# Kernel tuning notes

Hardware: AMD Instinct MI355X
Metric: run time of the kernel (lower is better)

The kernel has to match this reference:

```python
import jax, jax.numpy as jnp
import numpy as np

EMB = 1024
HEADS = 8
BUCKET = 64      # bucket_size
N_HASHES = 8


def setup_inputs() -> dict:
    key = jax.random.key(0)
    k0, k1, k2, k3, k4 = jax.random.split(key, 5)
    b, t, e = 2, 4096, EMB
    dh = e // HEADS
    n_buckets = t // BUCKET
    s = 1.0 / np.sqrt(e)
    return {
        "x": jax.random.normal(k0, (b, t, e), jnp.float32),
        "w_qk": jax.random.normal(k1, (e, e), jnp.float32) * s,
        "w_v": jax.random.normal(k2, (e, e), jnp.float32) * s,
        "w_out": jax.random.normal(k3, (e, e), jnp.float32) * s,
        "b_out": jnp.zeros((e,), jnp.float32),
        # LSH random rotations (shared across the batch, as in the TF module
        # with random_rotations_per_head=False): (dim_head, n_hashes, n_buckets//2)
        "rotations": jax.random.normal(k4, (dh, N_HASHES, n_buckets // 2), jnp.float32),
    }


def _lsh_attention(qk, v, rotations):
    # qk, v: (B, t, d) with B = batch*heads
    B, t, d = qk.shape
    nh = N_HASHES
    bucket = BUCKET
    n_buckets = t // bucket
    n_bins = n_buckets

    # ---- hash vectors ----
    rotated = jnp.einsum('btf,fhi->bhti', qk, rotations)      # (B, nh, t, nb/2)
    rotated = jnp.concatenate([rotated, -rotated], axis=-1)   # (B, nh, t, nb)
    buckets = jnp.argmax(rotated, axis=-1)                    # (B, nh, t)
    offsets = (jnp.arange(nh) * n_buckets)[None, :, None]
    buckets = (buckets + offsets).reshape(B, nh * t)          # (B, nh*t)

    # ---- sort by (bucket, position) ----
    ticker = jnp.arange(nh * t)
    buckets_and_t = t * buckets + (ticker % t)[None, :]
    sticker = jnp.argsort(buckets_and_t, axis=-1, stable=True)    # sort permutation
    undo_sort = jnp.argsort(sticker, axis=-1, stable=True)
    st = sticker % t                                              # token indices

    sqk = jnp.take_along_axis(qk, st[:, :, None], axis=1)         # (B, nh*t, d)
    sv = jnp.take_along_axis(v, st[:, :, None], axis=1)

    bq_t = st.reshape(B, nh * n_bins, bucket)
    bqk = sqk.reshape(B, nh * n_bins, bucket, d)
    bv = sv.reshape(B, nh * n_bins, bucket, d)

    bq = bqk
    # tf.math.l2_normalize with default epsilon 1e-12
    sq = jnp.maximum(jnp.sum(bqk * bqk, axis=-1, keepdims=True), 1e-12)
    bk = bqk * jax.lax.rsqrt(sq)

    def look_one_back(x):
        # x: (B, nh*n_bins, bucket[, d]) -> concat previous bin along window axis
        x1 = x.reshape((B, nh, n_bins) + x.shape[2:])
        x_extra = jnp.concatenate([x1[:, :, 1:2], x1[:, :, :-1]], axis=2)
        x_extra = x_extra.reshape(x.shape)
        return jnp.concatenate([x, x_extra], axis=2)

    bk = look_one_back(bk)        # (B, nh*n_bins, 2*bucket, d)
    bv = look_one_back(bv)
    bkv_t = look_one_back(bq_t)   # (B, nh*n_bins, 2*bucket)

    scale = d ** (-0.5)
    dots = jnp.einsum('bhie,bhje->bhij', bq * scale, bk)  # (B, nh*n_bins, bucket, 2*bucket)

    # self-attention mask (token attending to itself gets -1e5)
    self_mask = (bq_t[:, :, :, None] == bkv_t[:, :, None, :]).astype(dots.dtype)
    dots = dots * (1.0 - self_mask) + self_mask * (-1e5)

    dots_logsumexp = jax.scipy.special.logsumexp(dots, axis=-1, keepdims=True)
    probs = jnp.exp(dots - dots_logsumexp)
    bo = jnp.einsum('buij,buje->buie', probs, bv)          # (B, nh*n_bins, bucket, d)

    so = bo.reshape(B, nh * t, d)
    slogits = dots_logsumexp.reshape(B, nh * t)

    # unsort back to original token order
    o = jnp.take_along_axis(so, undo_sort[:, :, None], axis=1)
    logits = jnp.take_along_axis(slogits, undo_sort, axis=1)

    # combine the n_hashes rounds with softmax over per-round logsumexp logits
    o = o.reshape(B, nh, t, d)
    logits = logits.reshape(B, nh, t, 1)
    w = jnp.exp(logits - jax.scipy.special.logsumexp(logits, axis=1, keepdims=True))
    return jnp.sum(o * w, axis=1)  # (B, t, d)


def reference(x, w_qk, w_v, w_out, b_out, rotations):
    b, t, e = x.shape
    h = HEADS
    dh = e // h
    qk = x @ w_qk
    v = x @ w_v

    def merge_heads(z):
        return z.reshape(b, t, h, dh).transpose(0, 2, 1, 3).reshape(b * h, t, dh)

    out = _lsh_attention(merge_heads(qk), merge_heads(v), rotations)
    out = out.reshape(b, h, t, dh).transpose(0, 2, 1, 3).reshape(b, t, e)
    return out @ w_out + b_out
```

## Files before the change

### kernel.cpp

```cpp
#include <hip/hip_runtime.h>
#include <hip/hip_bf16.h>
#include <math.h>

#define T_LEN 4096
#define EMBD 1024
#define DH 128
#define NHASH 8
#define NHEADS 8
#define FLAG_CAP 65536
#define GAP_THRESH 2e-3f

typedef __attribute__((ext_vector_type(8))) short short8;
typedef __attribute__((ext_vector_type(16))) float f32x16;

__device__ __forceinline__ int swz(int row, int col) {
    return (row << 7) + (col ^ ((row & 7) << 3));
}
__device__ __forceinline__ int swz64(int row, int col) {
    return row * 64 + (col ^ ((row & 7) << 3));
}
__device__ __forceinline__ unsigned cvtpk(float lo, float hi) {
    unsigned r;
    asm("v_cvt_pk_bf16_f32 %0, %1, %2" : "=v"(r) : "v"(lo), "v"(hi));
    return r;
}
__device__ __forceinline__ float bfu_lo(unsigned u) {
    union { unsigned x; float f; } c; c.x = u << 16; return c.f;
}
__device__ __forceinline__ float bfu_hi(unsigned u) {
    union { unsigned x; float f; } c; c.x = u & 0xffff0000u; return c.f;
}
__device__ __forceinline__ float bfus2f(unsigned short s) {
    union { unsigned x; float f; } c; c.x = ((unsigned)s) << 16; return c.f;
}

__global__ __launch_bounds__(256) void k_prep_x(
    const float* __restrict__ x, __hip_bfloat16* __restrict__ xh,
    __hip_bfloat16* __restrict__ xl)
{
    int gid = blockIdx.x * 256 + threadIdx.x;
    for (int i = gid; i < 2097152; i += 524288) {
        float4 f = reinterpret_cast<const float4*>(x)[i];
        unsigned h01 = cvtpk(f.x, f.y), h23 = cvtpk(f.z, f.w);
        float l0 = f.x - bfu_lo(h01), l1 = f.y - bfu_hi(h01);
        float l2 = f.z - bfu_lo(h23), l3 = f.w - bfu_hi(h23);
        reinterpret_cast<uint2*>(xh)[i] = make_uint2(h01, h23);
        reinterpret_cast<uint2*>(xl)[i] = make_uint2(cvtpk(l0, l1), cvtpk(l2, l3));
    }
}

__global__ __launch_bounds__(256) void k_prep_w(
    const float* __restrict__ w0, const float* __restrict__ w1,
    const float* __restrict__ w2, __hip_bfloat16* __restrict__ wT)
{
    __shared__ float tileT[64 * 65];
    const int mat = blockIdx.x >> 8;
    const int tile = blockIdx.x & 255;
    const int tr = tile >> 4, tc = tile & 15;
    const int k0 = tr * 64, n0c = tc * 64;
    const float* w = (mat == 0) ? w0 : (mat == 1) ? w1 : w2;
    __hip_bfloat16* th = wT + (size_t)mat * 2097152;
    __hip_bfloat16* tl = th + 1048576;
    const int tid = threadIdx.x;

    #pragma unroll
    for (int i = 0; i < 4; ++i) {
        int idx = tid + i * 256;
        int row = idx >> 4, c4 = (idx & 15) * 4;
        float4 f = *reinterpret_cast<const float4*>(
            w + (size_t)(k0 + row) * 1024 + n0c + c4);
        tileT[(c4 + 0) * 65 + row] = f.x;
        tileT[(c4 + 1) * 65 + row] = f.y;
        tileT[(c4 + 2) * 65 + row] = f.z;
        tileT[(c4 + 3) * 65 + row] = f.w;
    }
    __syncthreads();
    #pragma unroll
    for (int i = 0; i < 4; ++i) {
        int idx = tid + i * 256;
        int nl = idx >> 4, kc4 = (idx & 15) * 4;
        float v0 = tileT[nl * 65 + kc4 + 0];
        float v1 = tileT[nl * 65 + kc4 + 1];
        float v2 = tileT[nl * 65 + kc4 + 2];
        float v3 = tileT[nl * 65 + kc4 + 3];
        unsigned h01 = cvtpk(v0, v1), h23 = cvtpk(v2, v3);
        float l0 = v0 - bfu_lo(h01), l1 = v1 - bfu_hi(h01);
        float l2 = v2 - bfu_lo(h23), l3 = v3 - bfu_hi(h23);
        size_t o = (size_t)(n0c + nl) * 1024 + k0 + kc4;
        *reinterpret_cast<uint2*>(th + o) = make_uint2(h01, h23);
        *reinterpret_cast<uint2*>(tl + o) = make_uint2(cvtpk(l0, l1), cvtpk(l2, l3));
    }
}

__global__ __launch_bounds__(256) void k_prep_a(
    const float* __restrict__ attn, const float* __restrict__ Sbuf,
    __hip_bfloat16* __restrict__ ah, __hip_bfloat16* __restrict__ al)
{
    int gid = blockIdx.x * 256 + threadIdx.x;
    for (int i = gid; i < 2097152; i += 524288) {
        int r = i >> 8;
        int e4 = (i & 255) * 4;
        int b = r >> 12, t = r & 4095;
        int h = e4 >> 7, d = e4 & 127;
        size_t gi = (size_t)(b * NHEADS + h) * T_LEN + t;
        float4 f = *reinterpret_cast<const float4*>(attn + gi * DH + d);
        float S = Sbuf[gi];
        f.x /= S; f.y /= S; f.z /= S; f.w /= S;
        unsigned h01 = cvtpk(f.x, f.y), h23 = cvtpk(f.z, f.w);
        float l0 = f.x - bfu_lo(h01), l1 = f.y - bfu_hi(h01);
        float l2 = f.z - bfu_lo(h23), l3 = f.w - bfu_hi(h23);
        reinterpret_cast<uint2*>(ah)[i] = make_uint2(h01, h23);
        reinterpret_cast<uint2*>(al)[i] = make_uint2(cvtpk(l0, l1), cvtpk(l2, l3));
    }
}

template <int EPI>
__global__ __launch_bounds__(256, 3) void k_gemm(
    const __hip_bfloat16* __restrict__ Xh_g, const __hip_bfloat16* __restrict__ Xl_g,
    const __hip_bfloat16* __restrict__ Wh_g, const __hip_bfloat16* __restrict__ Wl_g,
    void* __restrict__ o1v, void* __restrict__ o2v,
    float* __restrict__ rsn, const float* __restrict__ bias)
{
    __shared__ char smem[49152];
    short* Wh = (short*)smem;
    short* Wl = (short*)(smem + 16384);
    short* Xh = (short*)(smem + 32768);
    short* Xl = (short*)(smem + 40960);

    const int tid = threadIdx.x;
    const int mt = blockIdx.x >> 3;
    const int nt = blockIdx.x & 7;
    const int m0 = mt * 64, n0 = nt * 128;

    const int wave = tid >> 6, lane = tid & 63;
    const int it = wave & 1, jt2 = wave >> 1;
    const int h5 = lane >> 5;
    const int m_loc = it * 32 + (lane & 31);

    f32x16 acc[2] = {};

    for (int ks = 0; ks < 16; ++ks) {
        const int k0 = ks * 64;
        __syncthreads();
        for (int u = tid; u < 512; u += 256) {
            int row = u >> 3, blk = u & 7;
            size_t src = (size_t)(m0 + row) * 1024 + k0 + blk * 8;
            int dst = swz64(row, blk * 8);
            *reinterpret_cast<int4*>(&Xh[dst]) = *reinterpret_cast<const int4*>(Xh_g + src);
            *reinterpret_cast<int4*>(&Xl[dst]) = *reinterpret_cast<const int4*>(Xl_g + src);
        }
        for (int u = tid; u < 1024; u += 256) {
            int row = u >> 3, blk = u & 7;
            size_t src = (size_t)(n0 + row) * 1024 + k0 + blk * 8;
            int dst = swz64(row, blk * 8);
            *reinterpret_cast<int4*>(&Wh[dst]) = *reinterpret_cast<const int4*>(Wh_g + src);
            *reinterpret_cast<int4*>(&Wl[dst]) = *reinterpret_cast<const int4*>(Wl_g + src);
        }
        __syncthreads();

        #pragma unroll
        for (int kt = 0; kt < 4; ++kt) {
            int xoff = swz64(m_loc, kt * 16 + h5 * 8);
            short8 xfh = *reinterpret_cast<const short8*>(&Xh[xoff]);
            short8 xfl = *reinterpret_cast<const short8*>(&Xl[xoff]);
            #pragma unroll
            for (int jj = 0; jj < 2; ++jj) {
                int rowN = (jt2 * 2 + jj) * 32 + (lane & 31);
                int woff = swz64(rowN, kt * 16 + h5 * 8);
                short8 wfh = *reinterpret_cast<const short8*>(&Wh[woff]);
                short8 wfl = *reinterpret_cast<const short8*>(&Wl[woff]);
                acc[jj] = __builtin_amdgcn_mfma_f32_32x32x16_bf16(wfh, xfh, acc[jj], 0, 0, 0);
                acc[jj] = __builtin_amdgcn_mfma_f32_32x32x16_bf16(wfl, xfh, acc[jj], 0, 0, 0);
                acc[jj] = __builtin_amdgcn_mfma_f32_32x32x16_bf16(wfh, xfl, acc[jj], 0, 0, 0);
            }
        }
    }
    __syncthreads();

    float* osc = (float*)smem;
    #pragma unroll
    for (int jj = 0; jj < 2; ++jj) {
        int jt = jt2 * 2 + jj;
        #pragma unroll
        for (int r2 = 0; r2 < 16; ++r2) {
            int n = jt * 32 + (r2 & 3) + ((r2 >> 2) << 3) + (h5 << 2);
            osc[m_loc * 128 + (n ^ (m_loc & 28))] = acc[jj][r2];
        }
    }
    __syncthreads();

    #pragma unroll
    for (int w = 0; w < 8; ++w) {
        int lin = w * 256 + tid;
        int rowm = lin >> 5;
        int c4 = (lin & 31) * 4;
        float4 v4 = *reinterpret_cast<float4*>(&osc[rowm * 128 + (c4 ^ (rowm & 28))]);
        int r = m0 + rowm;
        if constexpr (EPI == 0) {
            float ss = v4.x * v4.x + v4.y * v4.y + v4.z * v4.z + v4.w * v4.w;
            #pragma unroll
            for (int mm = 1; mm < 32; mm <<= 1) ss += __shfl_xor(ss, mm);
            float rs = 1.0f / sqrtf(fmaxf(ss, 1e-12f));
            int b = r >> 12, t = r & 4095;
            int h = n0 >> 7;
            size_t base = ((size_t)(b * NHEADS + h) * T_LEN + t) * DH + c4;
            unsigned h01 = cvtpk(v4.x, v4.y), h23 = cvtpk(v4.z, v4.w);
            float l0 = v4.x - bfu_lo(h01), l1 = v4.y - bfu_hi(h01);
            float l2 = v4.z - bfu_lo(h23), l3 = v4.w - bfu_hi(h23);
            *reinterpret_cast<uint2*>((__hip_bfloat16*)o1v + base) = make_uint2(h01, h23);
            *reinterpret_cast<uint2*>((__hip_bfloat16*)o2v + base) =
                make_uint2(cvtpk(l0, l1), cvtpk(l2, l3));
            if ((lin & 31) == 0)
                rsn[(size_t)(b * NHEADS + h) * T_LEN + t] = rs;
        } else if constexpr (EPI == 1) {
            int b = r >> 12, t = r & 4095;
            int n = n0 + c4;
            int h = n >> 7, d = n & 127;
            size_t base = ((size_t)(b * NHEADS + h) * T_LEN + t) * DH + d;
            *reinterpret_cast<uint2*>((__hip_bfloat16*)o1v + base) =
                make_uint2(cvtpk(v4.x, v4.y), cvtpk(v4.z, v4.w));
        } else {
            int n = n0 + c4;
            float4 o;
            o.x = v4.x + bias[n + 0]; o.y = v4.y + bias[n + 1];
            o.z = v4.z + bias[n + 2]; o.w = v4.w + bias[n + 3];
            *reinterpret_cast<float4*>((float*)o1v + (size_t)r * 1024 + n) = o;
        }
    }
}

__global__ __launch_bounds__(256) void k_hash2f(
    const __hip_bfloat16* __restrict__ qkh, const __hip_bfloat16* __restrict__ qkl,
    const float* __restrict__ rot, unsigned* __restrict__ bucketArr,
    unsigned* __restrict__ counter, unsigned* __restrict__ flaglist)
{
    __shared__ float qs[8][EMBD];
    const int tok0 = blockIdx.x * 8;
    const int tid = threadIdx.x;
    const int j = 4 * tid;
    const int h = j >> 7, d = j & 127;

    #pragma unroll
    for (int tk = 0; tk < 8; ++tk) {
        int row = tok0 + tk;
        int b = row >> 12, t = row & 4095;
        size_t base = ((size_t)(b * NHEADS + h) * T_LEN + t) * DH + d;
        ushort4 h4 = *reinterpret_cast<const ushort4*>(qkh + base);
        ushort4 l4 = *reinterpret_cast<const ushort4*>(qkl + base);
        qs[tk][j + 0] = bfus2f(h4.x) + bfus2f(l4.x);
        qs[tk][j + 1] = bfus2f(h4.y) + bfus2f(l4.y);
        qs[tk][j + 2] = bfus2f(h4.z) + bfus2f(l4.z);
        qs[tk][j + 3] = bfus2f(h4.w) + bfus2f(l4.w);
    }
    __syncthreads();

    const int r = tid >> 5, i = tid & 31;
    const float* rp = rot + r * 32 + i;
    for (int hh = 0; hh < NHEADS; ++hh) {
        float acc[8] = {};
        for (int f = 0; f < DH; ++f) {
            float rv = rp[(size_t)f * 256];
            #pragma unroll
            for (int tk = 0; tk < 8; ++tk)
                acc[tk] = fmaf(qs[tk][hh * DH + f], rv, acc[tk]);
        }
        #pragma unroll
        for (int tk = 0; tk < 8; ++tk) {
            float v, v2; int idx;
            float a = acc[tk];
            if (a >= 0.0f) { v = a; idx = i; v2 = -a; }
            else           { v = -a; idx = i + 32; v2 = a; }
            #pragma unroll
            for (int m = 1; m < 32; m <<= 1) {
                float ov = __shfl_xor(v, m);
                int oi = __shfl_xor(idx, m);
                float ov2 = __shfl_xor(v2, m);
                bool owin = (ov > v) || (ov == v && oi < idx);
                float lv1 = owin ? v : ov;
                float wv2 = owin ? ov2 : v2;
                if (owin) { v = ov; idx = oi; }
                v2 = fmaxf(lv1, wv2);
            }
            if (i == 0) {
                int row = tok0 + tk;
                int b = row >> 12, t = row & 4095;
                int B = b * NHEADS + hh;
                bucketArr[((size_t)B * NHASH + r) * T_LEN + t] = (unsigned)idx;
                if (v - v2 < GAP_THRESH) {
                    unsigned p = atomicAdd(counter, 1u);
                    if (p < FLAG_CAP)
                        flaglist[p] = ((unsigned)B << 15) | ((unsigned)r << 12) | (unsigned)t;
                }
            }
        }
    }
}

__global__ __launch_bounds__(256) void k_fixup(
    const float* __restrict__ x, const float* __restrict__ wqk,
    const float* __restrict__ rot, const unsigned* __restrict__ counter,
    const unsigned* __restrict__ flaglist, unsigned* __restrict__ bucketArr)
{
    __shared__ float xsf[EMBD];
    __shared__ double qk64p[2][DH];
    __shared__ double vals[64];
    unsigned n = *counter;
    if (n > FLAG_CAP) n = FLAG_CAP;
    for (unsigned item = blockIdx.x; item < n; item += gridDim.x) {
        unsigned pk = flaglist[item];
        int t = pk & 4095, r = (pk >> 12) & 7, B = pk >> 15;
        int b = B >> 3, h = B & 7;
        reinterpret_cast<float4*>(xsf)[threadIdx.x] =
            reinterpret_cast<const float4*>(x + (size_t)(b * T_LEN + t) * EMBD)[threadIdx.x];
        __syncthreads();
        {
            int d = threadIdx.x & 127, gh = threadIdx.x >> 7;
            double a = 0.0;
            const float* wp = wqk + h * DH + d;
            const int e0 = gh << 9;
            for (int e = e0; e < e0 + 512; ++e)
                a = fma((double)xsf[e], (double)wp[(size_t)e * EMBD], a);
            qk64p[gh][d] = a;
        }
        __syncthreads();
        if (threadIdx.x < 32) {
            const float* rp = rot + r * 32 + threadIdx.x;
            double acc2 = 0.0;
            for (int f = 0; f < DH; ++f)
                acc2 = fma(qk64p[0][f] + qk64p[1][f], (double)rp[(size_t)f * 256], acc2);
            vals[threadIdx.x] = acc2;
            vals[threadIdx.x + 32] = -acc2;
        }
        __syncthreads();
        if (threadIdx.x == 0) {
            double best = vals[0]; int bi = 0;
            for (int u = 1; u < 64; ++u)
                if (vals[u] > best) { best = vals[u]; bi = u; }
            bucketArr[((size_t)B * NHASH + r) * T_LEN + t] = (unsigned)bi;
        }
        __syncthreads();
    }
}

__global__ __launch_bounds__(64) void k_sort(
    const unsigned* __restrict__ bucketArr, unsigned* __restrict__ st)
{
    __shared__ unsigned short bkt[T_LEN];
    __shared__ unsigned hist[64][64];
    __shared__ unsigned bstart[64];
    const int B = blockIdx.x >> 3, r = blockIdx.x & 7;
    const unsigned* src = bucketArr + ((size_t)B * NHASH + r) * T_LEN;
    const int tid = threadIdx.x;

    for (int k = tid; k < T_LEN; k += 64) bkt[k] = (unsigned short)src[k];
    for (int k = tid; k < 64 * 64; k += 64) (&hist[0][0])[k] = 0;
    __syncthreads();
    {
        const int base = tid * 64;
        for (int k = 0; k < 64; ++k) hist[tid][bkt[base + k]]++;
    }
    __syncthreads();
    {
        unsigned tot = 0;
        for (int c = 0; c < 64; ++c) tot += hist[c][tid];
        bstart[tid] = tot;
    }
    __syncthreads();
    if (tid == 0) {
        unsigned run = 0;
        for (int q = 0; q < 64; ++q) { unsigned c = bstart[q]; bstart[q] = run; run += c; }
    }
    __syncthreads();
    {
        unsigned run = bstart[tid];
        for (int c = 0; c < 64; ++c) { unsigned h = hist[c][tid]; hist[c][tid] = run; run += h; }
    }
    __syncthreads();
    {
        unsigned* dst = st + ((size_t)B * NHASH + r) * T_LEN;
        const int base = tid * 64;
        for (int k = 0; k < 64; ++k) {
            unsigned bb2 = bkt[base + k];
            unsigned p = hist[tid][bb2]++;
            dst[p] = (unsigned)(base + k);
        }
    }
}

__global__ __launch_bounds__(256, 3) void k_bin_pv(
    const __hip_bfloat16* __restrict__ qkh, const __hip_bfloat16* __restrict__ qkl,
    const __hip_bfloat16* __restrict__ vb, const float* __restrict__ rsn,
    const unsigned* __restrict__ st, float* __restrict__ Mbuf,
    float* __restrict__ Sbuf, float* __restrict__ attn, int rnd)
{
    __shared__ short Kh[128 * 128];
    __shared__ unsigned short Pb[64 * 128];
    __shared__ int ktok[128];
    __shared__ float rs_l[128];
    __shared__ float red4b[2][2][2][32];
    __shared__ float mrow[64];
    __shared__ float abrow[64][2];

    const int tid = threadIdx.x;
    const int c = blockIdx.x & 63;
    const int B = blockIdx.x >> 6;
    const unsigned* stp = st + ((size_t)B * NHASH + rnd) * T_LEN;

    if (tid < 128) {
        int cc = (tid < 64) ? c : (c == 0 ? 1 : c - 1);
        int tok = (int)stp[cc * 64 + (tid & 63)];
        ktok[tid] = tok;
        rs_l[tid] = rsn[(size_t)B * T_LEN + tok];
    }
    __syncthreads();

    for (int u = tid; u < 128 * 16; u += 256) {
        int row = u >> 4, blk = u & 15;
        *reinterpret_cast<int4*>(&Kh[swz(row, blk * 8)]) =
            *reinterpret_cast<const int4*>(qkh + ((size_t)B * T_LEN + ktok[row]) * DH + blk * 8);
    }

    const int wave = tid >> 6, lane = tid & 63;
    const int it = wave & 1, jt2 = wave >> 1;
    const int h5 = lane >> 5;
    const int i_loc = it * 32 + (lane & 31);
    const int qtok_i = ktok[i_loc];
    short8 qfh[8], qfl[8];
    {
        size_t qoff = ((size_t)B * T_LEN + qtok_i) * DH + (h5 << 3);
        #pragma unroll
        for (int kt = 0; kt < 8; ++kt) {
            qfh[kt] = *reinterpret_cast<const short8*>(qkh + qoff + kt * 16);
            qfl[kt] = *reinterpret_cast<const short8*>(qkl + qoff + kt * 16);
        }
    }
    __syncthreads();

    const float scale = 0.08838834764831845f;
    float p2[2][16];
    #pragma unroll
    for (int jj = 0; jj < 2; ++jj) {
        int jt = jt2 * 2 + jj;
        f32x16 acc = {};
        #pragma unroll
        for (int kt = 0; kt < 8; ++kt) {
            int so = swz(jt * 32 + (lane & 31), kt * 16 + (h5 << 3));
            short8 afh = *reinterpret_cast<const short8*>(&Kh[so]);
            acc = __builtin_amdgcn_mfma_f32_32x32x16_bf16(afh, qfh[kt], acc, 0, 0, 0);
            acc = __builtin_amdgcn_mfma_f32_32x32x16_bf16(afh, qfl[kt], acc, 0, 0, 0);
        }
        #pragma unroll
        for (int r2 = 0; r2 < 16; ++r2) {
            int jl = (r2 & 3) + ((r2 >> 2) << 3) + (h5 << 2);
            int jf = jt * 32 + jl;
            float s = acc[r2] * (scale * rs_l[jf]);
            p2[jj][r2] = (ktok[jf] == qtok_i) ? -1e5f : s;
        }
    }

    float mloc = p2[0][0];
    #pragma unroll
    for (int jj = 0; jj < 2; ++jj)
        #pragma unroll
        for (int r2 = 0; r2 < 16; ++r2) mloc = fmaxf(mloc, p2[jj][r2]);
    red4b[it][jt2][h5][lane & 31] = mloc;
    __syncthreads();
    if (tid < 64) {
        int it2 = tid >> 5, i = tid & 31;
        mrow[tid] = fmaxf(fmaxf(red4b[it2][0][0][i], red4b[it2][0][1][i]),
                          fmaxf(red4b[it2][1][0][i], red4b[it2][1][1][i]));
    }
    __syncthreads();

    const float mi = mrow[i_loc];
    float sloc = 0.f;
    #pragma unroll
    for (int jj = 0; jj < 2; ++jj)
        #pragma unroll
        for (int r2 = 0; r2 < 16; ++r2) {
            float p = __expf(p2[jj][r2] - mi);
            p2[jj][r2] = p;
            sloc += p;
        }
    red4b[it][jt2][h5][lane & 31] = sloc;
    __syncthreads();

    if (tid < 64) {
        int it2 = tid >> 5, i = tid & 31;
        float sr = red4b[it2][0][0][i] + red4b[it2][0][1][i] +
                   red4b[it2][1][0][i] + red4b[it2][1][1][i];
        float m = mrow[tid];
        size_t gi = (size_t)B * T_LEN + ktok[tid];
        float aw, bw;
        if (rnd == 0) {
            Mbuf[gi] = m; Sbuf[gi] = sr;
            aw = 0.f; bw = 1.f;
        } else {
            float Mold = Mbuf[gi];
            float Mnew = fmaxf(Mold, m);
            aw = __expf(Mold - Mnew);
            bw = __expf(m - Mnew);
            Sbuf[gi] = Sbuf[gi] * aw + sr * bw;
            Mbuf[gi] = Mnew;
        }
        abrow[tid][0] = aw; abrow[tid][1] = bw;
    }
    #pragma unroll
    for (int jj = 0; jj < 2; ++jj) {
        int jt = jt2 * 2 + jj;
        #pragma unroll
        for (int q = 0; q < 4; ++q) {
            int jhalf = jt * 16 + 4 * q + 2 * h5;
            unsigned pk0 = cvtpk(p2[jj][4 * q + 0], p2[jj][4 * q + 1]);
            unsigned pk1 = cvtpk(p2[jj][4 * q + 2], p2[jj][4 * q + 3]);
            *reinterpret_cast<unsigned*>(&Pb[jhalf * 128 + i_loc * 2]) = pk0;
            *reinterpret_cast<unsigned*>(&Pb[(jhalf + 1) * 128 + i_loc * 2]) = pk1;
        }
    }
    {
        int j2 = tid >> 1, dbase = (tid & 1) * 64;
        const __hip_bfloat16* vrow = vb + ((size_t)B * T_LEN + ktok[j2]) * DH + dbase;
        #pragma unroll
        for (int mch = 0; mch < 8; ++mch) {
            short8 vv = *reinterpret_cast<const short8*>(vrow + mch * 8);
            #pragma unroll
            for (int e = 0; e < 8; ++e)
                Kh[swz(dbase + mch * 8 + e, j2)] = vv[e];
        }
    }
    __syncthreads();

    f32x16 oacc[4] = {};
    #pragma unroll
    for (int jj = 0; jj < 2; ++jj) {
        int jt = jt2 * 2 + jj;
        #pragma unroll
        for (int ks = 0; ks < 2; ++ks) {
            int jb0 = jt * 32 + ks * 16 + h5 * 8;
            union Pack { unsigned u[4]; short8 v; } ph;
            #pragma unroll
            for (int m = 0; m < 4; ++m)
                ph.u[m] = *reinterpret_cast<const unsigned*>(
                    &Pb[((jb0 >> 1) + m) * 128 + i_loc * 2]);
            #pragma unroll
            for (int dt = 0; dt < 4; ++dt) {
                short8 af = *reinterpret_cast<const short8*>(
                    &Kh[swz(dt * 32 + (lane & 31), jb0)]);
                oacc[dt] = __builtin_amdgcn_mfma_f32_32x32x16_bf16(af, ph.v, oacc[dt], 0, 0, 0);
            }
        }
    }
    __syncthreads();

    float* osc = reinterpret_cast<float*>(Kh);
    if (jt2 == 1) {
        #pragma unroll
        for (int dt = 0; dt < 4; ++dt)
            #pragma unroll
            for (int r2 = 0; r2 < 16; ++r2) {
                int d = dt * 32 + (r2 & 3) + ((r2 >> 2) << 3) + (h5 << 2);
                osc[i_loc * 128 + (d ^ (i_loc & 28))] = oacc[dt][r2];
            }
    }
    __syncthreads();
    if (jt2 == 0) {
        #pragma unroll
        for (int dt = 0; dt < 4; ++dt)
            #pragma unroll
            for (int r2 = 0; r2 < 16; ++r2) {
                int d = dt * 32 + (r2 & 3) + ((r2 >> 2) << 3) + (h5 << 2);
                int a = i_loc * 128 + (d ^ (i_loc & 28));
                osc[a] += oacc[dt][r2];
            }
    }
    __syncthreads();

    #pragma unroll
    for (int w = 0; w < 8; ++w) {
        int lin = w * 256 + tid;
        int rowq = lin >> 5;
        int d0 = (lin & 31) * 4;
        float4 sv4 = *reinterpret_cast<float4*>(&osc[rowq * 128 + (d0 ^ (rowq & 28))]);
        float* gp = attn + ((size_t)B * T_LEN + ktok[rowq]) * DH + d0;
        if (rnd == 0) {
            *reinterpret_cast<float4*>(gp) = sv4;
        } else {
            float aw = abrow[rowq][0], bw = abrow[rowq][1];
            float4 g = *reinterpret_cast<float4*>(gp);
            g.x = g.x * aw + sv4.x * bw;
            g.y = g.y * aw + sv4.y * bw;
            g.z = g.z * aw + sv4.z * bw;
            g.w = g.w * aw + sv4.w * bw;
            *reinterpret_cast<float4*>(gp) = g;
        }
    }
}

extern "C" void kernel_launch(void* const* d_in, const int* in_sizes, int n_in,
                              void* d_out, int out_size, void* d_ws, size_t ws_size,
                              hipStream_t stream)
{
    const float* x    = (const float*)d_in[0];
    const float* wqk  = (const float*)d_in[1];
    const float* wv   = (const float*)d_in[2];
    const float* wout = (const float*)d_in[3];
    const float* bout = (const float*)d_in[4];
    const float* rot  = (const float*)d_in[5];
    float* out = (float*)d_out;

    char* ws = (char*)d_ws;
    __hip_bfloat16* qkh       = (__hip_bfloat16*)(ws);
    __hip_bfloat16* qkl       = (__hip_bfloat16*)(ws + 16777216);
    __hip_bfloat16* vb        = (__hip_bfloat16*)(ws + 33554432);
    float*          attn      = (float*)        (ws + 50331648);
    __hip_bfloat16* xh        = (__hip_bfloat16*)(ws + 50331648);
    __hip_bfloat16* xl        = (__hip_bfloat16*)(ws + 67108864);
    unsigned*       bucketArr = (unsigned*)     (ws + 83886080);
    unsigned*       st        = (unsigned*)     (ws + 85983232);
    float*          Mbuf      = (float*)        (ws + 88080384);
    float*          Sbuf      = (float*)        (ws + 88342528);
    float*          rsn       = (float*)        (ws + 90439680);
    unsigned*       counter   = (unsigned*)     (ws + 90701824);
    unsigned*       flaglist  = (unsigned*)     (ws + 90705920);
    __hip_bfloat16* wT        = (__hip_bfloat16*)(ws + 90968064);
    __hip_bfloat16* ah        = qkh;
    __hip_bfloat16* al        = qkl;

    hipMemsetAsync(counter, 0, 4, stream);
    k_prep_x<<<2048, 256, 0, stream>>>(x, xh, xl);
    k_prep_w<<<768, 256, 0, stream>>>(wqk, wv, wout, wT);
    k_gemm<0><<<1024, 256, 0, stream>>>(xh, xl, wT, wT + 1048576,
                                        qkh, qkl, rsn, nullptr);
    k_gemm<1><<<1024, 256, 0, stream>>>(xh, xl, wT + 2097152, wT + 3145728,
                                        vb, nullptr, nullptr, nullptr);
    k_hash2f<<<1024, 256, 0, stream>>>(qkh, qkl, rot, bucketArr, counter, flaglist);
    k_fixup<<<1024, 256, 0, stream>>>(x, wqk, rot, counter, flaglist, bucketArr);
    k_sort<<<128, 64, 0, stream>>>(bucketArr, st);
    for (int r = 0; r < NHASH; ++r)
        k_bin_pv<<<1024, 256, 0, stream>>>(qkh, qkl, vb, rsn, st, Mbuf, Sbuf, attn, r);
    k_prep_a<<<2048, 256, 0, stream>>>(attn, Sbuf, ah, al);
    k_gemm<2><<<1024, 256, 0, stream>>>(ah, al, wT + 4194304, wT + 5242880,
                                        out, nullptr, nullptr, bout);
}
```

Baseline: 810.6 us.

## Compute LSH hash rotations with split-bf16 MFMA instead of scalar FMA

Replaces the scalar-FMA hashing kernel with an MFMA GEMM over 64-token tiles against a bf16 hi/lo split of the transposed rotation matrix. A small new kernel prepares the split rotations, and the argmax with its top-two gap check runs from an LDS scratch tile. The aim is to move the hash projection onto matrix cores. Precision changes slightly because the lo*lo term is dropped, though near-tie cases are still flagged for the fp64 fixup.

```diff
diff --git a/kernel.cpp b/kernel.cpp
--- a/kernel.cpp
+++ b/kernel.cpp
@@ -90,6 +90,24 @@
         *reinterpret_cast<uint2*>(th + o) = make_uint2(h01, h23);
         *reinterpret_cast<uint2*>(tl + o) = make_uint2(cvtpk(l0, l1), cvtpk(l2, l3));
     }
+}
+
+__global__ __launch_bounds__(256) void k_prep_rot(
+    const float* __restrict__ rot, __hip_bfloat16* __restrict__ rth,
+    __hip_bfloat16* __restrict__ rtl)
+{
+    int gid = blockIdx.x * 256 + threadIdx.x;
+    int ri = gid >> 5, f0 = (gid & 31) * 4;
+    float v0 = rot[(size_t)(f0 + 0) * 256 + ri];
+    float v1 = rot[(size_t)(f0 + 1) * 256 + ri];
+    float v2 = rot[(size_t)(f0 + 2) * 256 + ri];
+    float v3 = rot[(size_t)(f0 + 3) * 256 + ri];
+    unsigned h01 = cvtpk(v0, v1), h23 = cvtpk(v2, v3);
+    float l0 = v0 - bfu_lo(h01), l1 = v1 - bfu_hi(h01);
+    float l2 = v2 - bfu_lo(h23), l3 = v3 - bfu_hi(h23);
+    size_t o = (size_t)ri * 128 + f0;
+    *reinterpret_cast<uint2*>(rth + o) = make_uint2(h01, h23);
+    *reinterpret_cast<uint2*>(rtl + o) = make_uint2(cvtpk(l0, l1), cvtpk(l2, l3));
 }
 
 __global__ __launch_bounds__(256) void k_prep_a(
@@ -229,69 +247,100 @@
     }
 }
 
-__global__ __launch_bounds__(256) void k_hash2f(
-    const __hip_bfloat16* __restrict__ qkh, const __hip_bfloat16* __restrict__ qkl,
-    const float* __restrict__ rot, unsigned* __restrict__ bucketArr,
-    unsigned* __restrict__ counter, unsigned* __restrict__ flaglist)
-{
-    __shared__ float qs[8][EMBD];
-    const int tok0 = blockIdx.x * 8;
+__global__ __launch_bounds__(256, 2) void k_hash_mfma(
+    const __hip_bfloat16* __restrict__ Xh_g, const __hip_bfloat16* __restrict__ Xl_g,
+    const __hip_bfloat16* __restrict__ Wh_g, const __hip_bfloat16* __restrict__ Wl_g,
+    unsigned* __restrict__ bucketArr, unsigned* __restrict__ counter,
+    unsigned* __restrict__ flaglist)
+{
+    __shared__ char smem[81920];
+    short* Wh = (short*)smem;
+    short* Wl = (short*)(smem + 32768);
+    short* Xh = (short*)(smem + 65536);
+    short* Xl = (short*)(smem + 73728);
+
     const int tid = threadIdx.x;
-    const int j = 4 * tid;
-    const int h = j >> 7, d = j & 127;
-
-    #pragma unroll
-    for (int tk = 0; tk < 8; ++tk) {
-        int row = tok0 + tk;
-        int b = row >> 12, t = row & 4095;
-        size_t base = ((size_t)(b * NHEADS + h) * T_LEN + t) * DH + d;
-        ushort4 h4 = *reinterpret_cast<const ushort4*>(qkh + base);
-        ushort4 l4 = *reinterpret_cast<const ushort4*>(qkl + base);
-        qs[tk][j + 0] = bfus2f(h4.x) + bfus2f(l4.x);
-        qs[tk][j + 1] = bfus2f(h4.y) + bfus2f(l4.y);
-        qs[tk][j + 2] = bfus2f(h4.z) + bfus2f(l4.z);
-        qs[tk][j + 3] = bfus2f(h4.w) + bfus2f(l4.w);
-    }
-    __syncthreads();
-
-    const int r = tid >> 5, i = tid & 31;
-    const float* rp = rot + r * 32 + i;
-    for (int hh = 0; hh < NHEADS; ++hh) {
-        float acc[8] = {};
-        for (int f = 0; f < DH; ++f) {
-            float rv = rp[(size_t)f * 256];
-            #pragma unroll
-            for (int tk = 0; tk < 8; ++tk)
-                acc[tk] = fmaf(qs[tk][hh * DH + f], rv, acc[tk]);
-        }
-        #pragma unroll
-        for (int tk = 0; tk < 8; ++tk) {
-            float v, v2; int idx;
-            float a = acc[tk];
-            if (a >= 0.0f) { v = a; idx = i; v2 = -a; }
-            else           { v = -a; idx = i + 32; v2 = a; }
-            #pragma unroll
-            for (int m = 1; m < 32; m <<= 1) {
-                float ov = __shfl_xor(v, m);
-                int oi = __shfl_xor(idx, m);
-                float ov2 = __shfl_xor(v2, m);
-                bool owin = (ov > v) || (ov == v && oi < idx);
-                float lv1 = owin ? v : ov;
-                float wv2 = owin ? ov2 : v2;
-                if (owin) { v = ov; idx = oi; }
-                v2 = fmaxf(lv1, wv2);
+    const int m0 = blockIdx.x * 64;
+    const int wave = tid >> 6, lane = tid & 63;
+    const int it = wave & 1, jt2 = wave >> 1;
+    const int h5 = lane >> 5;
+    const int m_loc = it * 32 + (lane & 31);
+
+    f32x16 acc[4] = {};
+
+    for (int ks = 0; ks < 2; ++ks) {
+        const int k0 = ks * 64;
+        __syncthreads();
+        for (int u = tid; u < 512; u += 256) {
+            int row = u >> 3, blk = u & 7;
+            size_t src = (size_t)(m0 + row) * 128 + k0 + blk * 8;
+            int dst = swz64(row, blk * 8);
+            *reinterpret_cast<int4*>(&Xh[dst]) = *reinterpret_cast<const int4*>(Xh_g + src);
+            *reinterpret_cast<int4*>(&Xl[dst]) = *reinterpret_cast<const int4*>(Xl_g + src);
+        }
+        for (int u = tid; u < 2048; u += 256) {
+            int row = u >> 3, blk = u & 7;
+            size_t src = (size_t)row * 128 + k0 + blk * 8;
+            int dst = swz64(row, blk * 8);
+            *reinterpret_cast<int4*>(&Wh[dst]) = *reinterpret_cast<const int4*>(Wh_g + src);
+            *reinterpret_cast<int4*>(&Wl[dst]) = *reinterpret_cast<const int4*>(Wl_g + src);
+        }
+        __syncthreads();
+
+        #pragma unroll
+        for (int kt = 0; kt < 4; ++kt) {
+            int xoff = swz64(m_loc, kt * 16 + h5 * 8);
+            short8 xfh = *reinterpret_cast<const short8*>(&Xh[xoff]);
+            short8 xfl = *reinterpret_cast<const short8*>(&Xl[xoff]);
+            #pragma unroll
+            for (int jj = 0; jj < 4; ++jj) {
+                int rowN = (jt2 * 4 + jj) * 32 + (lane & 31);
+                int woff = swz64(rowN, kt * 16 + h5 * 8);
+                short8 wfh = *reinterpret_cast<const short8*>(&Wh[woff]);
+                short8 wfl = *reinterpret_cast<const short8*>(&Wl[woff]);
+                acc[jj] = __builtin_amdgcn_mfma_f32_32x32x16_bf16(wfh, xfh, acc[jj], 0, 0, 0);
+                acc[jj] = __builtin_amdgcn_mfma_f32_32x32x16_bf16(wfl, xfh, acc[jj], 0, 0, 0);
+                acc[jj] = __builtin_amdgcn_mfma_f32_32x32x16_bf16(wfh, xfl, acc[jj], 0, 0, 0);
             }
-            if (i == 0) {
-                int row = tok0 + tk;
-                int b = row >> 12, t = row & 4095;
-                int B = b * NHEADS + hh;
-                bucketArr[((size_t)B * NHASH + r) * T_LEN + t] = (unsigned)idx;
-                if (v - v2 < GAP_THRESH) {
-                    unsigned p = atomicAdd(counter, 1u);
-                    if (p < FLAG_CAP)
-                        flaglist[p] = ((unsigned)B << 15) | ((unsigned)r << 12) | (unsigned)t;
-                }
-            }
+        }
+    }
+    __syncthreads();
+
+    float* osc = (float*)smem;
+    #pragma unroll
+    for (int jj = 0; jj < 4; ++jj) {
+        int jt = jt2 * 4 + jj;
+        #pragma unroll
+        for (int r2 = 0; r2 < 16; ++r2) {
+            int n = jt * 32 + (r2 & 3) + ((r2 >> 2) << 3) + (h5 << 2);
+            osc[m_loc * 256 + (n ^ (m_loc & 28))] = acc[jj][r2];
+        }
+    }
+    __syncthreads();
+
+    #pragma unroll
+    for (int p = 0; p < 2; ++p) {
+        int pair = tid * 2 + p;
+        int row = pair >> 3, r = pair & 7;
+        float best = -1e30f, second = -1e30f;
+        int bi = 0;
+        for (int i = 0; i < 32; ++i) {
+            float cv = osc[row * 256 + ((r * 32 + i) ^ (row & 28))];
+            if (cv > best) { second = best; best = cv; bi = i; }
+            else if (cv > second) second = cv;
+        }
+        for (int i = 0; i < 32; ++i) {
+            float cv = -osc[row * 256 + ((r * 32 + i) ^ (row & 28))];
+            if (cv > best) { second = best; best = cv; bi = i + 32; }
+            else if (cv > second) second = cv;
+        }
+        int gr = m0 + row;
+        int B = gr >> 12, t = gr & 4095;
+        bucketArr[((size_t)B * NHASH + r) * T_LEN + t] = (unsigned)bi;
+        if (best - second < GAP_THRESH) {
+            unsigned pp = atomicAdd(counter, 1u);
+            if (pp < FLAG_CAP)
+                flaglist[pp] = ((unsigned)B << 15) | ((unsigned)r << 12) | (unsigned)t;
         }
     }
 }
@@ -623,17 +672,21 @@
     unsigned*       counter   = (unsigned*)     (ws + 90701824);
     unsigned*       flaglist  = (unsigned*)     (ws + 90705920);
     __hip_bfloat16* wT        = (__hip_bfloat16*)(ws + 90968064);
+    __hip_bfloat16* rotTh     = (__hip_bfloat16*)(ws + 103550976);
+    __hip_bfloat16* rotTl     = (__hip_bfloat16*)(ws + 103616512);
     __hip_bfloat16* ah        = qkh;
     __hip_bfloat16* al        = qkl;
 
     hipMemsetAsync(counter, 0, 4, stream);
     k_prep_x<<<2048, 256, 0, stream>>>(x, xh, xl);
     k_prep_w<<<768, 256, 0, stream>>>(wqk, wv, wout, wT);
+    k_prep_rot<<<32, 256, 0, stream>>>(rot, rotTh, rotTl);
     k_gemm<0><<<1024, 256, 0, stream>>>(xh, xl, wT, wT + 1048576,
                                         qkh, qkl, rsn, nullptr);
     k_gemm<1><<<1024, 256, 0, stream>>>(xh, xl, wT + 2097152, wT + 3145728,
                                         vb, nullptr, nullptr, nullptr);
-    k_hash2f<<<1024, 256, 0, stream>>>(qkh, qkl, rot, bucketArr, counter, flaglist);
+    k_hash_mfma<<<1024, 256, 0, stream>>>(qkh, qkl, rotTh, rotTl,
+                                          bucketArr, counter, flaglist);
     k_fixup<<<1024, 256, 0, stream>>>(x, wqk, rot, counter, flaglist, bucketArr);
     k_sort<<<128, 64, 0, stream>>>(bucketArr, st);
     for (int r = 0; r < NHASH; ++r)
```

Result: faster. 726.6 us (-10.4%).
